# Performance work log

Measured on AMD Instinct MI355X. Metric: run time of the kernel, lower is better.

## Reference

```python
import jax, jax.numpy as jnp
import numpy as np

B, T, D = 2, 2048, 1024
HEADS = 16
MEM = 512
HEAD_DIM = D // HEADS


def setup_inputs() -> dict:
    key = jax.random.key(0)
    k1, k2, k3, k4, k5 = jax.random.split(key, 5)
    x = jax.random.normal(k1, (B, T, D), dtype=jnp.float32)
    w_qkv = jax.random.normal(k2, (3 * D, D), dtype=jnp.float32) * (1.0 / np.sqrt(D))
    w_out = jax.random.normal(k3, (D, D), dtype=jnp.float32) * (1.0 / np.sqrt(D))
    b_out = jax.random.normal(k4, (D,), dtype=jnp.float32) * 0.01
    memory = jax.random.normal(k5, (MEM, D), dtype=jnp.float32)
    return {"x": x, "w_qkv": w_qkv, "w_out": w_out, "b_out": b_out, "memory": memory}


def reference(x, w_qkv, w_out, b_out, memory):
    b, t, d = x.shape
    h, hd = HEADS, HEAD_DIM
    scale = hd ** -0.5
    # QKV projection: [B,T,3D]
    qkv = jnp.einsum('btd,ed->bte', x, w_qkv)
    q, k, v = jnp.split(qkv, 3, axis=-1)
    # [B,H,T,hd]
    q = q.reshape(b, t, h, hd).transpose(0, 2, 1, 3)
    k = k.reshape(b, t, h, hd).transpose(0, 2, 1, 3)
    v = v.reshape(b, t, h, hd).transpose(0, 2, 1, 3)
    # memory K/V: [B,H,MEM,hd] (broadcast over batch)
    mem = memory.reshape(1, MEM, h, hd).transpose(0, 2, 1, 3)
    mem = jnp.broadcast_to(mem, (b, h, MEM, hd))
    k = jnp.concatenate([mem, k], axis=2)
    v = jnp.concatenate([mem, v], axis=2)
    # attention: scores [B,H,T,MEM+T]
    scores = jnp.einsum('bhqd,bhkd->bhqk', q, k) * scale
    weights = jax.nn.softmax(scores, axis=-1)
    out = jnp.einsum('bhqk,bhkd->bhqd', weights, v)
    out = out.transpose(0, 2, 1, 3).reshape(b, t, d)
    return jnp.einsum('btd,ed->bte', out, w_out) + b_out
```

## Files before the change

kernel.cpp:

```cpp
#include <hip/hip_runtime.h>
#include <hip/hip_bf16.h>
#include <stdint.h>

#define B_   2
#define T_   2048
#define D_   1024
#define H_   16
#define HD_  64
#define MEM_ 512
#define KV_  (MEM_ + T_)
#define NIT_ (KV_ / 64)

#define XN_   (4096 * 1024)
#define WQN_  (3072 * 1024)
#define WON_  (1024 * 1024)
#define MN_   (512 * 1024)

using bf16 = __bf16;
typedef __bf16 bf16x8 __attribute__((ext_vector_type(8)));
typedef float  f32x4  __attribute__((ext_vector_type(4)));
typedef short  s16x4  __attribute__((ext_vector_type(4)));

__device__ __forceinline__ f32x4 mfma16(bf16x8 a, bf16x8 b, f32x4 c) {
  return __builtin_amdgcn_mfma_f32_16x16x32_bf16(a, b, c, 0, 0, 0);
}
__device__ __forceinline__ f32x4 mfma16k16(s16x4 a, s16x4 b, f32x4 c) {
  return __builtin_amdgcn_mfma_f32_16x16x16bf16_1k(a, b, c, 0, 0, 0);
}

__device__ __forceinline__ void gl_lds16(const bf16* g, bf16* l) {
  __builtin_amdgcn_global_load_lds(
      (const __attribute__((address_space(1))) void*)g,
      (__attribute__((address_space(3))) void*)l, 16, 0, 0);
}

__device__ __forceinline__ unsigned short bf16_bits(float f) {
  bf16 h = (bf16)f;
  return __builtin_bit_cast(unsigned short, h);
}

__device__ __forceinline__ ushort4 pack4(f32x4 v) {
  ushort4 p;
  p.x = bf16_bits(v[0]); p.y = bf16_bits(v[1]);
  p.z = bf16_bits(v[2]); p.w = bf16_bits(v[3]);
  return p;
}

__global__ void convert_all(const float* __restrict__ x,
                            const float* __restrict__ wq,
                            const float* __restrict__ wo,
                            const float* __restrict__ mem,
                            bf16* __restrict__ xb, bf16* __restrict__ wqb,
                            bf16* __restrict__ wob, bf16* __restrict__ mem_k,
                            bf16* __restrict__ mem_vt) {
  size_t e = ((size_t)blockIdx.x * 256 + threadIdx.x) * 4;
  if (e < XN_) {
    f32x4 v = *(const f32x4*)(x + e);
    *(ushort4*)&xb[e] = pack4(v);
  } else if (e < XN_ + WQN_) {
    size_t o = e - XN_;
    f32x4 v = *(const f32x4*)(wq + o);
    *(ushort4*)&wqb[o] = pack4(v);
  } else if (e < XN_ + WQN_ + WON_) {
    size_t o = e - XN_ - WQN_;
    f32x4 v = *(const f32x4*)(wo + o);
    *(ushort4*)&wob[o] = pack4(v);
  } else {
    size_t o = e - XN_ - WQN_ - WON_;
    f32x4 v = *(const f32x4*)(mem + o);
    *(ushort4*)&mem_k[o] = pack4(v);
    int m = (int)(o >> 10), d = (int)(o & 1023);
#pragma unroll
    for (int j = 0; j < 4; j++)
      mem_vt[(size_t)(d + j) * MEM_ + m] = (bf16)v[j];
  }
}

template <int EPI, bool APLANE>
__global__ __launch_bounds__(256) void gemm_lds(
    const bf16* __restrict__ A, const bf16* __restrict__ W,
    const float* __restrict__ bias,
    bf16* __restrict__ q_ws, bf16* __restrict__ k_ws, bf16* __restrict__ vt_ws,
    float* __restrict__ Cout, int K) {
  __shared__ __align__(16) bf16 Als[128 * 32];
  __shared__ __align__(16) bf16 Bls[128 * 32];
  const int m0 = blockIdx.y * 128;
  const int n0 = blockIdx.x * 128;
  const int tid = threadIdx.x;
  const int w = tid >> 6;
  const int lane = tid & 63;
  const int lx = lane & 15;
  const int quad = lane >> 4;
  const int amb = (w & 1) * 64;
  const int bnb = (w >> 1) * 64;

  f32x4 acc[4][4];
#pragma unroll
  for (int i = 0; i < 4; i++)
#pragma unroll
    for (int j = 0; j < 4; j++) acc[i][j] = (f32x4){0.f, 0.f, 0.f, 0.f};

  for (int k0 = 0; k0 < K; k0 += 32) {
    __syncthreads();
#pragma unroll
    for (int i = 0; i < 2; i++) {
      int chunk = i * 256 + tid;
      int row = chunk >> 2, seg = chunk & 3;
      const bf16* ga;
      if constexpr (APLANE) {
        int c0 = k0 + seg * 8;
        int m = m0 + row;
        ga = A + ((size_t)((m >> 11) * H_ + (c0 >> 6)) * T_ + (m & 2047)) *
                     HD_ + (c0 & 63);
      } else {
        ga = A + (size_t)(m0 + row) * K + k0 + seg * 8;
      }
      gl_lds16(ga, &Als[i * 2048 + w * 512]);
      gl_lds16(W + (size_t)(n0 + row) * K + k0 + seg * 8,
               &Bls[i * 2048 + w * 512]);
    }
    __syncthreads();

    bf16x8 af[4], bfr[4];
#pragma unroll
    for (int mt = 0; mt < 4; mt++)
      af[mt] = *(const bf16x8*)&Als[(amb + mt * 16 + lx) * 32 + quad * 8];
#pragma unroll
    for (int nt = 0; nt < 4; nt++)
      bfr[nt] = *(const bf16x8*)&Bls[(bnb + nt * 16 + lx) * 32 + quad * 8];
#pragma unroll
    for (int mt = 0; mt < 4; mt++)
#pragma unroll
      for (int nt = 0; nt < 4; nt++)
        acc[mt][nt] = mfma16(af[mt], bfr[nt], acc[mt][nt]);
  }

  if (EPI == 0) {
#pragma unroll
    for (int mt = 0; mt < 4; mt++) {
      int mbase = m0 + amb + mt * 16 + quad * 4;
      int b = mbase >> 11;
      int t = mbase & 2047;
#pragma unroll
      for (int nt = 0; nt < 4; nt++) {
        int col = n0 + bnb + nt * 16 + lx;
        int which = col >> 10;
        int d = col & 1023;
        int h = d >> 6, hdi = d & 63;
        int bh = b * H_ + h;
        if (which == 0) {
#pragma unroll
          for (int r = 0; r < 4; r++)
            q_ws[((size_t)bh * T_ + t + r) * HD_ + hdi] = (bf16)acc[mt][nt][r];
        } else if (which == 1) {
#pragma unroll
          for (int r = 0; r < 4; r++)
            k_ws[((size_t)bh * T_ + t + r) * HD_ + hdi] = (bf16)acc[mt][nt][r];
        } else {
          *(ushort4*)&vt_ws[((size_t)bh * HD_ + hdi) * T_ + t] =
              pack4(acc[mt][nt]);
        }
      }
    }
  } else {
#pragma unroll
    for (int nt = 0; nt < 4; nt++) {
      int col = n0 + bnb + nt * 16 + lx;
      float bias_f = bias[col];
#pragma unroll
      for (int mt = 0; mt < 4; mt++) {
        int mbase = m0 + amb + mt * 16 + quad * 4;
#pragma unroll
        for (int r = 0; r < 4; r++)
          Cout[(size_t)(mbase + r) * D_ + col] = acc[mt][nt][r] + bias_f;
      }
    }
  }
}

__global__ __launch_bounds__(256, 2) void attn_kernel(
    bf16* __restrict__ q_ws, const bf16* __restrict__ k_ws,
    const bf16* __restrict__ vt_ws, const bf16* __restrict__ mem_k,
    const bf16* __restrict__ mem_vt) {
  __shared__ __align__(16) bf16 Kls[64][72];
  __shared__ __align__(16) bf16 Vls[64][72];
  const int tid = threadIdx.x;
  const int w = tid >> 6;
  const int lane = tid & 63;
  const int lx = lane & 15;
  const int quad = lane >> 4;
  const int bh = blockIdx.x & 31;
  const int qt = blockIdx.x >> 5;
  const int q0 = qt * 128 + w * 32;
  const int h = bh & 15;

  const int srow1 = tid >> 3, soff1 = (tid & 7) * 8;
  const int srow2 = (tid + 256) >> 3, soff2 = soff1;

  bf16* qbase = q_ws + ((size_t)bh * T_ + q0) * HD_;

  bf16x8 qf[2][2];
#pragma unroll
  for (int qg = 0; qg < 2; qg++)
#pragma unroll
    for (int hf = 0; hf < 2; hf++) {
      bf16x8 v = *(const bf16x8*)(qbase + (size_t)(qg * 16 + lx) * HD_ +
                                  hf * 32 + quad * 8);
#pragma unroll
      for (int i = 0; i < 8; i++)
        v[i] = (bf16)((float)v[i] * 0.125f);
      qf[qg][hf] = v;
    }

  const bf16* kplane = k_ws + (size_t)bh * T_ * HD_;
  const bf16* vtplane = vt_ws + (size_t)bh * HD_ * T_;
  const bf16* mkh = mem_k + h * HD_;
  const bf16* mvh = mem_vt + (size_t)h * HD_ * MEM_;

  f32x4 o[4][2];
#pragma unroll
  for (int mt = 0; mt < 4; mt++)
#pragma unroll
    for (int qg = 0; qg < 2; qg++) o[mt][qg] = (f32x4){0.f, 0.f, 0.f, 0.f};
  float lsum[2] = {0.f, 0.f};

  for (int it = 0; it < NIT_; it++) {
    const int kv0 = it * 64;
    const bool memPart = kv0 < MEM_;
    bf16x8 kr1, kr2, vr1, vr2;
    if (memPart) {
      kr1 = *(const bf16x8*)(mkh + (size_t)(kv0 + srow1) * D_ + soff1);
      kr2 = *(const bf16x8*)(mkh + (size_t)(kv0 + srow2) * D_ + soff2);
      vr1 = *(const bf16x8*)(mvh + (size_t)srow1 * MEM_ + kv0 + soff1);
      vr2 = *(const bf16x8*)(mvh + (size_t)srow2 * MEM_ + kv0 + soff2);
    } else {
      const int t0 = kv0 - MEM_;
      kr1 = *(const bf16x8*)(kplane + (size_t)(t0 + srow1) * HD_ + soff1);
      kr2 = *(const bf16x8*)(kplane + (size_t)(t0 + srow2) * HD_ + soff2);
      vr1 = *(const bf16x8*)(vtplane + (size_t)srow1 * T_ + t0 + soff1);
      vr2 = *(const bf16x8*)(vtplane + (size_t)srow2 * T_ + t0 + soff2);
    }
    __syncthreads();
    *(bf16x8*)&Kls[srow1][soff1] = kr1;
    *(bf16x8*)&Kls[srow2][soff2] = kr2;
    *(bf16x8*)&Vls[srow1][soff1] = vr1;
    *(bf16x8*)&Vls[srow2][soff2] = vr2;
    __syncthreads();

    f32x4 s[4][2];
#pragma unroll
    for (int g = 0; g < 4; g++) {
      bf16x8 ka0 = *(const bf16x8*)&Kls[g * 16 + lx][quad * 8];
      bf16x8 ka1 = *(const bf16x8*)&Kls[g * 16 + lx][32 + quad * 8];
#pragma unroll
      for (int qg = 0; qg < 2; qg++) {
        s[g][qg] = (f32x4){0.f, 0.f, 0.f, 0.f};
        s[g][qg] = mfma16(ka0, qf[qg][0], s[g][qg]);
        s[g][qg] = mfma16(ka1, qf[qg][1], s[g][qg]);
      }
    }

    s16x4 pb[2][4];
#pragma unroll
    for (int qg = 0; qg < 2; qg++) {
      float ps = 0.f;
#pragma unroll
      for (int g = 0; g < 4; g++) {
#pragma unroll
        for (int r = 0; r < 4; r++) {
          float p = __expf(s[g][qg][r]);
          ps += p;
          pb[qg][g][r] = (short)bf16_bits(p);
        }
      }
      lsum[qg] += ps;
    }

#pragma unroll
    for (int mt = 0; mt < 4; mt++) {
#pragma unroll
      for (int kk = 0; kk < 4; kk++) {
        s16x4 va = *(const s16x4*)&Vls[mt * 16 + lx][kk * 16 + quad * 4];
#pragma unroll
        for (int qg = 0; qg < 2; qg++)
          o[mt][qg] = mfma16k16(va, pb[qg][kk], o[mt][qg]);
      }
    }
  }

  float inv[2];
#pragma unroll
  for (int qg = 0; qg < 2; qg++) {
    float s2 = lsum[qg];
    s2 += __shfl_xor(s2, 16);
    s2 += __shfl_xor(s2, 32);
    inv[qg] = 1.f / s2;
  }

#pragma unroll
  for (int qg = 0; qg < 2; qg++) {
#pragma unroll
    for (int mt = 0; mt < 4; mt++) {
      f32x4 ov;
#pragma unroll
      for (int r = 0; r < 4; r++) ov[r] = o[mt][qg][r] * inv[qg];
      *(ushort4*)(qbase + (size_t)(qg * 16 + lx) * HD_ + mt * 16 + quad * 4)
          = pack4(ov);
    }
  }
}

extern "C" void kernel_launch(void* const* d_in, const int* in_sizes, int n_in,
                              void* d_out, int out_size, void* d_ws,
                              size_t ws_size, hipStream_t stream) {
  const float* x      = (const float*)d_in[0];
  const float* w_qkv  = (const float*)d_in[1];
  const float* w_out  = (const float*)d_in[2];
  const float* b_out  = (const float*)d_in[3];
  const float* memory = (const float*)d_in[4];

  char* ws = (char*)d_ws;
  bf16* q_ws   = (bf16*)(ws);
  bf16* k_ws   = (bf16*)(ws + (8u << 20));
  bf16* vt_ws  = (bf16*)(ws + (16u << 20));
  bf16* mem_k  = (bf16*)(ws + (24u << 20));
  bf16* mem_vt = (bf16*)(ws + (25u << 20));
  bf16* wob    = (bf16*)(ws + (26u << 20));
  char* outc = (char*)d_out;
  bf16* xb  = (bf16*)(outc);
  bf16* wqb = (bf16*)(outc + (8u << 20));
  float* out = (float*)d_out;

  convert_all<<<dim3(8704), dim3(256), 0, stream>>>(
      x, w_qkv, w_out, memory, xb, wqb, wob, mem_k, mem_vt);
  gemm_lds<0, false><<<dim3(24, 32), dim3(256), 0, stream>>>(
      xb, wqb, nullptr, q_ws, k_ws, vt_ws, nullptr, 1024);
  attn_kernel<<<dim3(512), dim3(256), 0, stream>>>(
      q_ws, k_ws, vt_ws, mem_k, mem_vt);
  gemm_lds<1, true><<<dim3(8, 32), dim3(256), 0, stream>>>(
      q_ws, wob, b_out, nullptr, nullptr, nullptr, out, 1024);
}
```

Baseline: 223.6 us.

## Split attention KV range across two blocks and merge partial outputs

The attention kernel now launches twice as many blocks. Each block processes half of the key/value sequence and writes an unnormalized bf16 partial output plus its row-sum to scratch. A new merge kernel adds the two partials and normalizes them into the buffer read by the output projection. Launch bounds are raised to allow more blocks per CU. The aim is better occupancy and parallelism on a grid that was previously only about two blocks per CU. The cost is an extra kernel launch, extra global traffic for the partials, and rounding the unnormalized partials to bf16.

Result: slower. 228.9 us (+2.4%).

```diff
diff --git a/kernel.cpp b/kernel.cpp
--- a/kernel.cpp
+++ b/kernel.cpp
@@ -10,11 +10,11 @@
 #define MEM_ 512
 #define KV_  (MEM_ + T_)
 #define NIT_ (KV_ / 64)
+#define HITER (NIT_ / 2)
 
 #define XN_   (4096 * 1024)
 #define WQN_  (3072 * 1024)
 #define WON_  (1024 * 1024)
-#define MN_   (512 * 1024)
 
 using bf16 = __bf16;
 typedef __bf16 bf16x8 __attribute__((ext_vector_type(8)));
@@ -178,10 +178,11 @@
   }
 }
 
-__global__ __launch_bounds__(256, 2) void attn_kernel(
-    bf16* __restrict__ q_ws, const bf16* __restrict__ k_ws,
+__global__ __launch_bounds__(256, 4) void attn_kernel(
+    const bf16* __restrict__ q_ws, const bf16* __restrict__ k_ws,
     const bf16* __restrict__ vt_ws, const bf16* __restrict__ mem_k,
-    const bf16* __restrict__ mem_vt) {
+    const bf16* __restrict__ mem_vt, bf16* __restrict__ opart,
+    float* __restrict__ lpart) {
   __shared__ __align__(16) bf16 Kls[64][72];
   __shared__ __align__(16) bf16 Vls[64][72];
   const int tid = threadIdx.x;
@@ -190,14 +191,15 @@
   const int lx = lane & 15;
   const int quad = lane >> 4;
   const int bh = blockIdx.x & 31;
-  const int qt = blockIdx.x >> 5;
+  const int qt = (blockIdx.x >> 5) & 15;
+  const int half = blockIdx.x >> 9;
   const int q0 = qt * 128 + w * 32;
   const int h = bh & 15;
 
   const int srow1 = tid >> 3, soff1 = (tid & 7) * 8;
   const int srow2 = (tid + 256) >> 3, soff2 = soff1;
 
-  bf16* qbase = q_ws + ((size_t)bh * T_ + q0) * HD_;
+  const bf16* qbase = q_ws + ((size_t)bh * T_ + q0) * HD_;
 
   bf16x8 qf[2][2];
 #pragma unroll
@@ -224,7 +226,8 @@
     for (int qg = 0; qg < 2; qg++) o[mt][qg] = (f32x4){0.f, 0.f, 0.f, 0.f};
   float lsum[2] = {0.f, 0.f};
 
-  for (int it = 0; it < NIT_; it++) {
+  const int it0 = half * HITER;
+  for (int it = it0; it < it0 + HITER; it++) {
     const int kv0 = it * 64;
     const bool memPart = kv0 < MEM_;
     bf16x8 kr1, kr2, vr1, vr2;
@@ -288,26 +291,37 @@
     }
   }
 
-  float inv[2];
 #pragma unroll
   for (int qg = 0; qg < 2; qg++) {
     float s2 = lsum[qg];
     s2 += __shfl_xor(s2, 16);
     s2 += __shfl_xor(s2, 32);
-    inv[qg] = 1.f / s2;
-  }
-
-#pragma unroll
-  for (int qg = 0; qg < 2; qg++) {
-#pragma unroll
-    for (int mt = 0; mt < 4; mt++) {
-      f32x4 ov;
-#pragma unroll
-      for (int r = 0; r < 4; r++) ov[r] = o[mt][qg][r] * inv[qg];
-      *(ushort4*)(qbase + (size_t)(qg * 16 + lx) * HD_ + mt * 16 + quad * 4)
-          = pack4(ov);
-    }
-  }
+    if (quad == 0)
+      lpart[(size_t)half * 65536 + (size_t)bh * T_ + q0 + qg * 16 + lx] = s2;
+  }
+
+  bf16* obase = opart + (size_t)half * 4194304 + ((size_t)bh * T_ + q0) * HD_;
+#pragma unroll
+  for (int qg = 0; qg < 2; qg++)
+#pragma unroll
+    for (int mt = 0; mt < 4; mt++)
+      *(ushort4*)(obase + (size_t)(qg * 16 + lx) * HD_ + mt * 16 + quad * 4) =
+          pack4(o[mt][qg]);
+}
+
+__global__ void merge_kernel(const bf16* __restrict__ opart,
+                             const float* __restrict__ lpart,
+                             bf16* __restrict__ q_ws) {
+  size_t i8 = ((size_t)blockIdx.x * 256 + threadIdx.x) * 8;
+  size_t row = i8 >> 6;
+  float inv = 1.f / (lpart[row] + lpart[65536 + row]);
+  bf16x8 a = *(const bf16x8*)(opart + i8);
+  bf16x8 b = *(const bf16x8*)(opart + 4194304 + i8);
+  bf16x8 r;
+#pragma unroll
+  for (int j = 0; j < 8; j++)
+    r[j] = (bf16)(((float)a[j] + (float)b[j]) * inv);
+  *(bf16x8*)(q_ws + i8) = r;
 }
 
 extern "C" void kernel_launch(void* const* d_in, const int* in_sizes, int n_in,
@@ -326,17 +340,20 @@
   bf16* mem_k  = (bf16*)(ws + (24u << 20));
   bf16* mem_vt = (bf16*)(ws + (25u << 20));
   bf16* wob    = (bf16*)(ws + (26u << 20));
+  float* lpart = (float*)(ws + (28u << 20));
   char* outc = (char*)d_out;
-  bf16* xb  = (bf16*)(outc);
-  bf16* wqb = (bf16*)(outc + (8u << 20));
+  bf16* xb    = (bf16*)(outc);
+  bf16* wqb   = (bf16*)(outc + (8u << 20));
+  bf16* opart = (bf16*)(outc);
   float* out = (float*)d_out;
 
   convert_all<<<dim3(8704), dim3(256), 0, stream>>>(
       x, w_qkv, w_out, memory, xb, wqb, wob, mem_k, mem_vt);
   gemm_lds<0, false><<<dim3(24, 32), dim3(256), 0, stream>>>(
       xb, wqb, nullptr, q_ws, k_ws, vt_ws, nullptr, 1024);
-  attn_kernel<<<dim3(512), dim3(256), 0, stream>>>(
-      q_ws, k_ws, vt_ws, mem_k, mem_vt);
+  attn_kernel<<<dim3(1024), dim3(256), 0, stream>>>(
+      q_ws, k_ws, vt_ws, mem_k, mem_vt, opart, lpart);
+  merge_kernel<<<dim3(2048), dim3(256), 0, stream>>>(opart, lpart, q_ws);
   gemm_lds<1, true><<<dim3(8, 32), dim3(256), 0, stream>>>(
       q_ws, wob, b_out, nullptr, nullptr, nullptr, out, 1024);
 }
```
